# Performance work log

Measured on AMD Instinct MI355X. Metric: run time of the kernel, lower is better.

## Reference

```python
import jax, jax.numpy as jnp
import numpy as np

N_PARENTS = 8
CHILDREN_PER_PARENT = 7
N_CHILDREN = N_PARENTS * CHILDREN_PER_PARENT  # 56 leaf classes
TOTAL_NODES = N_PARENTS + N_CHILDREN          # 64
BATCH = 262144


def _build_state_space():
    """Faithful port of generate_state_space for levels==2.

    Row 0 is the all-zero root state; then for each parent, one parent-only
    row, followed by one (parent, child) row per child. Shape [65, 64].
    """
    S = np.zeros((TOTAL_NODES + 1, TOTAL_NODES), dtype=np.float32)
    recorded = np.zeros(TOTAL_NODES)
    ii = 1
    for c in range(N_CHILDREN):
        p = N_CHILDREN + c // CHILDREN_PER_PARENT  # parent ids 56..63
        if recorded[p] == 0:
            S[ii, p] = 1.0
            recorded[p] = 1
            ii += 1
        S[ii, p] = 1.0
        S[ii, c] = 1.0
        ii += 1
    assert ii == TOTAL_NODES + 1, 'Invalid State Space'
    return jnp.asarray(S)


def setup_inputs() -> dict:
    key = jax.random.key(0)
    k1, k2 = jax.random.split(key)
    pred_label = jax.random.normal(k1, (BATCH, TOTAL_NODES), dtype=jnp.float32)
    gt_label = jax.random.randint(k2, (BATCH,), 0, N_CHILDREN, dtype=jnp.int32)
    return {
        'pred_label': pred_label,
        'gt_label': gt_label,
        'state_space': _build_state_space(),
    }


def reference(pred_label, gt_label, state_space):
    # index[s, b] = <state_space row s, pred_label[b]>  -> [S+1, B]
    index = state_space @ pred_label.T
    joint = jnp.exp(index)                      # [S+1, B]
    z = jnp.sum(joint, axis=0)                  # [B] partition function
    # Vectorized replacement of the per-sample Python loop:
    # rows of the state space that contain the ground-truth node.
    mask = state_space[:, gt_label] > 0         # [S+1, B]
    marginal = jnp.sum(jnp.where(mask, joint, jnp.zeros((), joint.dtype)), axis=0)  # [B]
    loss = -jnp.log(marginal / z)               # [B]
    return jnp.mean(loss)
```

## Files before the change

### kernel.cpp

```cpp
#include <hip/hip_runtime.h>


#define THREADS 256
#define WROWS   32
#define RPB     (4 * WROWS)
#define STRIDE  68

__device__ __forceinline__ float elem(const float4& v, int j) {
    return j == 0 ? v.x : j == 1 ? v.y : j == 2 ? v.z : v.w;
}

__global__ void __launch_bounds__(THREADS) tree_loss_partial(
    const float* __restrict__ pred,
    const int*   __restrict__ gt,
    float*       __restrict__ partial,
    int rows)
{
    __shared__ float lds[4 * WROWS * STRIDE];
    __shared__ float wsum[4];

    const int t = threadIdx.x;
    const int w = t >> 6;
    const int l = t & 63;
    const int waveRowBase = blockIdx.x * RPB + w * WROWS;
    float* e_base = &lds[w * WROWS * STRIDE];

    const float4* p4 = (const float4*)pred + (size_t)waveRowBase * 16;
    const bool full = (waveRowBase + WROWS <= rows);
    float4 v[8];
    #pragma unroll
    for (int i = 0; i < 8; ++i) {
        const int f = i * 64 + l;
        v[i] = (full || waveRowBase + (f >> 4) < rows)
                 ? p4[f] : make_float4(0.f, 0.f, 0.f, 0.f);
    }
    #pragma unroll
    for (int i = 0; i < 8; ++i) {
        const int f   = i * 64 + l;
        const int row = f >> 4;
        const int c4  = (f & 15) << 2;
        float4 ef;
        ef.x = __expf(v[i].x); ef.y = __expf(v[i].y);
        ef.z = __expf(v[i].z); ef.w = __expf(v[i].w);
        *(float4*)(e_base + row * STRIDE + c4) = ef;
    }

    const int r  = l & 31;
    const int hi = l >> 5;
    const float* e = e_base + r * STRIDE;

    float4 ch[7];
    #pragma unroll
    for (int k = 0; k < 7; ++k)
        ch[k] = *(const float4*)(e + hi * 28 + 4 * k);
    const float4 pv = *(const float4*)(e + 56 + 4 * hi);

    float zh = 0.f;
    #pragma unroll
    for (int p = 0; p < 4; ++p) {
        float s = 1.f;
        #pragma unroll
        for (int c = 0; c < 7; ++c) {
            const int idx = p * 7 + c;
            s += elem(ch[idx >> 2], idx & 3);
        }
        zh += elem(pv, p) * s;
    }
    const float zo = __shfl_xor(zh, 32);

    const int  rowg  = waveRowBase + r;
    const bool valid = (rowg < rows);
    float loss = 0.f;
    if (hi == 0 && valid) {
        const int g = gt[rowg];
        const float z = 1.f + zh + zo;
        const float m = e[g] * e[56 + g / 7];
        loss = __logf(z / m);
    }

    #pragma unroll
    for (int off = 32; off; off >>= 1) loss += __shfl_xor(loss, off);
    if (l == 0) wsum[w] = loss;
    __syncthreads();
    if (t == 0) partial[blockIdx.x] = wsum[0] + wsum[1] + wsum[2] + wsum[3];
}

__global__ void __launch_bounds__(256) tree_loss_final(
    const float* __restrict__ partial, int n,
    float* __restrict__ out, float inv)
{
    float s = 0.0f;
    for (int i = threadIdx.x; i < n; i += 256) s += partial[i];
    #pragma unroll
    for (int off = 32; off; off >>= 1) s += __shfl_xor(s, off);
    __shared__ float w[4];
    const int lane = threadIdx.x & 63;
    const int wv   = threadIdx.x >> 6;
    if (lane == 0) w[wv] = s;
    __syncthreads();
    if (threadIdx.x == 0) out[0] = (w[0] + w[1] + w[2] + w[3]) * inv;
}

extern "C" void kernel_launch(void* const* d_in, const int* in_sizes, int n_in,
                              void* d_out, int out_size, void* d_ws, size_t ws_size,
                              hipStream_t stream) {
    const float* pred = (const float*)d_in[0];
    const int*   gt   = (const int*)d_in[1];
    float* out     = (float*)d_out;
    float* partial = (float*)d_ws;
    const int rows = in_sizes[1];

    const int blocks = (rows + RPB - 1) / RPB;
    tree_loss_partial<<<blocks, THREADS, 0, stream>>>(pred, gt, partial, rows);
    tree_loss_final<<<1, 256, 0, stream>>>(partial, blocks, out, 1.0f / (float)rows);
}
```

Before: 22.00 us.

## Fuse final reduction via last-block atomic counter with grid-stride persistent blocks

Replaces the two-kernel scheme (per-block partials plus a separate final reduction kernel) with a single persistent kernel of 1024 blocks that grid-stride over 32-row tiles. The last block to finish, detected through an atomic counter, sums the partials and writes the mean. This removes one kernel launch and reduces the number of partials, at the cost of a memset before the launch and a serialized tail in the last block. The grid-stride loop also processes tiles serially per wave, which may reduce memory-level parallelism compared to one tile per wave.

Measured after the change: 53.24 us. +142.0%, slower.

```diff
diff --git a/kernel.cpp b/kernel.cpp
--- a/kernel.cpp
+++ b/kernel.cpp
@@ -3,18 +3,20 @@
 
 #define THREADS 256
 #define WROWS   32
-#define RPB     (4 * WROWS)
 #define STRIDE  68
+#define BLOCKS  1024
 
 __device__ __forceinline__ float elem(const float4& v, int j) {
     return j == 0 ? v.x : j == 1 ? v.y : j == 2 ? v.z : v.w;
 }
 
-__global__ void __launch_bounds__(THREADS) tree_loss_partial(
+__global__ void __launch_bounds__(THREADS) tree_loss(
     const float* __restrict__ pred,
     const int*   __restrict__ gt,
     float*       __restrict__ partial,
-    int rows)
+    int*         __restrict__ counter,
+    float*       __restrict__ out,
+    int rows, float inv)
 {
     __shared__ float lds[4 * WROWS * STRIDE];
     __shared__ float wsum[4];
@@ -22,83 +24,93 @@
     const int t = threadIdx.x;
     const int w = t >> 6;
     const int l = t & 63;
-    const int waveRowBase = blockIdx.x * RPB + w * WROWS;
     float* e_base = &lds[w * WROWS * STRIDE];
 
-    const float4* p4 = (const float4*)pred + (size_t)waveRowBase * 16;
-    const bool full = (waveRowBase + WROWS <= rows);
-    float4 v[8];
-    #pragma unroll
-    for (int i = 0; i < 8; ++i) {
-        const int f = i * 64 + l;
-        v[i] = (full || waveRowBase + (f >> 4) < rows)
-                 ? p4[f] : make_float4(0.f, 0.f, 0.f, 0.f);
-    }
-    #pragma unroll
-    for (int i = 0; i < 8; ++i) {
-        const int f   = i * 64 + l;
-        const int row = f >> 4;
-        const int c4  = (f & 15) << 2;
-        float4 ef;
-        ef.x = __expf(v[i].x); ef.y = __expf(v[i].y);
-        ef.z = __expf(v[i].z); ef.w = __expf(v[i].w);
-        *(float4*)(e_base + row * STRIDE + c4) = ef;
-    }
+    const int nwaves = (int)gridDim.x * 4;
+    const int ntiles = (rows + WROWS - 1) / WROWS;
 
-    const int r  = l & 31;
-    const int hi = l >> 5;
-    const float* e = e_base + r * STRIDE;
+    float acc = 0.f;
+    for (int tile = (int)blockIdx.x * 4 + w; tile < ntiles; tile += nwaves) {
+        const int waveRowBase = tile * WROWS;
+        const bool full = (waveRowBase + WROWS <= rows);
 
-    float4 ch[7];
-    #pragma unroll
-    for (int k = 0; k < 7; ++k)
-        ch[k] = *(const float4*)(e + hi * 28 + 4 * k);
-    const float4 pv = *(const float4*)(e + 56 + 4 * hi);
+        const float4* p4 = (const float4*)pred + (size_t)waveRowBase * 16;
+        float4 v[8];
+        #pragma unroll
+        for (int i = 0; i < 8; ++i) {
+            const int f = i * 64 + l;
+            v[i] = (full || waveRowBase + (f >> 4) < rows)
+                     ? p4[f] : make_float4(0.f, 0.f, 0.f, 0.f);
+        }
+        #pragma unroll
+        for (int i = 0; i < 8; ++i) {
+            const int f   = i * 64 + l;
+            const int row = f >> 4;
+            const int c4  = (f & 15) << 2;
+            float4 ef;
+            ef.x = __expf(v[i].x); ef.y = __expf(v[i].y);
+            ef.z = __expf(v[i].z); ef.w = __expf(v[i].w);
+            *(float4*)(e_base + row * STRIDE + c4) = ef;
+        }
 
-    float zh = 0.f;
-    #pragma unroll
-    for (int p = 0; p < 4; ++p) {
-        float s = 1.f;
+        const int r  = l & 31;
+        const int hi = l >> 5;
+        const float* e = e_base + r * STRIDE;
+
+        float4 ch[7];
         #pragma unroll
-        for (int c = 0; c < 7; ++c) {
-            const int idx = p * 7 + c;
-            s += elem(ch[idx >> 2], idx & 3);
+        for (int k = 0; k < 7; ++k)
+            ch[k] = *(const float4*)(e + hi * 28 + 4 * k);
+        const float4 pv = *(const float4*)(e + 56 + 4 * hi);
+
+        float zh = 0.f;
+        #pragma unroll
+        for (int p = 0; p < 4; ++p) {
+            float s = 1.f;
+            #pragma unroll
+            for (int c = 0; c < 7; ++c) {
+                const int idx = p * 7 + c;
+                s += elem(ch[idx >> 2], idx & 3);
+            }
+            zh += elem(pv, p) * s;
         }
-        zh += elem(pv, p) * s;
-    }
-    const float zo = __shfl_xor(zh, 32);
+        const float zo = __shfl_xor(zh, 32);
 
-    const int  rowg  = waveRowBase + r;
-    const bool valid = (rowg < rows);
-    float loss = 0.f;
-    if (hi == 0 && valid) {
-        const int g = gt[rowg];
-        const float z = 1.f + zh + zo;
-        const float m = e[g] * e[56 + g / 7];
-        loss = __logf(z / m);
+        const int  rowg  = waveRowBase + r;
+        const bool valid = (rowg < rows);
+        if (hi == 0 && valid) {
+            const int g = gt[rowg];
+            const float z = 1.f + zh + zo;
+            const float m = e[g] * e[56 + g / 7];
+            acc += __logf(z / m);
+        }
     }
 
     #pragma unroll
-    for (int off = 32; off; off >>= 1) loss += __shfl_xor(loss, off);
-    if (l == 0) wsum[w] = loss;
+    for (int off = 32; off; off >>= 1) acc += __shfl_xor(acc, off);
+    if (l == 0) wsum[w] = acc;
     __syncthreads();
-    if (t == 0) partial[blockIdx.x] = wsum[0] + wsum[1] + wsum[2] + wsum[3];
-}
 
-__global__ void __launch_bounds__(256) tree_loss_final(
-    const float* __restrict__ partial, int n,
-    float* __restrict__ out, float inv)
-{
-    float s = 0.0f;
-    for (int i = threadIdx.x; i < n; i += 256) s += partial[i];
-    #pragma unroll
-    for (int off = 32; off; off >>= 1) s += __shfl_xor(s, off);
-    __shared__ float w[4];
-    const int lane = threadIdx.x & 63;
-    const int wv   = threadIdx.x >> 6;
-    if (lane == 0) w[wv] = s;
-    __syncthreads();
-    if (threadIdx.x == 0) out[0] = (w[0] + w[1] + w[2] + w[3]) * inv;
+    if (w == 0) {
+        int old = 0;
+        if (t == 0) {
+            const float b = wsum[0] + wsum[1] + wsum[2] + wsum[3];
+            __hip_atomic_store(&partial[blockIdx.x], b,
+                               __ATOMIC_RELEASE, __HIP_MEMORY_SCOPE_AGENT);
+            old = __hip_atomic_fetch_add(counter, 1,
+                                         __ATOMIC_ACQ_REL, __HIP_MEMORY_SCOPE_AGENT);
+        }
+        old = __shfl(old, 0);
+        if (old == (int)gridDim.x - 1) {
+            float s = 0.f;
+            for (int i = l; i < (int)gridDim.x; i += 64)
+                s += __hip_atomic_load(&partial[i],
+                                       __ATOMIC_ACQUIRE, __HIP_MEMORY_SCOPE_AGENT);
+            #pragma unroll
+            for (int off = 32; off; off >>= 1) s += __shfl_xor(s, off);
+            if (l == 0) out[0] = s * inv;
+        }
+    }
 }
 
 extern "C" void kernel_launch(void* const* d_in, const int* in_sizes, int n_in,
@@ -106,11 +118,13 @@
                               hipStream_t stream) {
     const float* pred = (const float*)d_in[0];
     const int*   gt   = (const int*)d_in[1];
-    float* out     = (float*)d_out;
-    float* partial = (float*)d_ws;
+    float* out = (float*)d_out;
     const int rows = in_sizes[1];
 
-    const int blocks = (rows + RPB - 1) / RPB;
-    tree_loss_partial<<<blocks, THREADS, 0, stream>>>(pred, gt, partial, rows);
-    tree_loss_final<<<1, 256, 0, stream>>>(partial, blocks, out, 1.0f / (float)rows);
+    float* partial = (float*)d_ws;
+    int*   counter = (int*)((char*)d_ws + 4096);
+
+    hipMemsetAsync(counter, 0, sizeof(int), stream);
+    tree_loss<<<BLOCKS, THREADS, 0, stream>>>(
+        pred, gt, partial, counter, out, rows, 1.0f / (float)rows);
 }
```

## Stage pred tiles straight into swizzled LDS and double-buffer per wave

Applied to the files above, without the earlier changes.

The partial kernel now copies pred rows from global memory straight into LDS with global_load_lds dwordx4. The LDS layout is XOR-swizzled instead of padded, and each wave handles two 32-row tiles, using vmcnt waits so computing the first tile overlaps the second tile's load. The loss is now computed in the log domain (log z minus the two logits), so only the exps needed for z are evaluated after the LDS read. Each wave writes its own partial sum, which removes the block barrier, and the final reduction is widened to 1024 threads to handle four times as many partials. This relies on hand-written waitcnt counts and on the gfx950 LDS-load path being correct. Rows past the end are not loaded and are masked out afterwards.

New measurement: 20.08 us. -8.7%, faster.

```diff
diff --git a/kernel.cpp b/kernel.cpp
--- a/kernel.cpp
+++ b/kernel.cpp
@@ -3,11 +3,65 @@
 
 #define THREADS 256
 #define WROWS   32
-#define RPB     (4 * WROWS)
-#define STRIDE  68
+#define RPB     256
 
 __device__ __forceinline__ float elem(const float4& v, int j) {
     return j == 0 ? v.x : j == 1 ? v.y : j == 2 ? v.z : v.w;
+}
+
+__device__ __forceinline__ void stage_tile(const float* __restrict__ pred,
+                                           int rowBase, float* ldsReg,
+                                           int l, int rows) {
+    #pragma unroll
+    for (int i = 0; i < 8; ++i) {
+        const int f   = i * 64 + l;
+        const int rr  = f >> 4;
+        const int sc  = (f & 15) ^ (rr & 7);
+        const int row = rowBase + rr;
+        if (row < rows) {
+            const float* src = pred + (size_t)row * 64 + sc * 4;
+            __builtin_amdgcn_global_load_lds(
+                (const __attribute__((address_space(1))) float*)src,
+                (__attribute__((address_space(3))) float*)(ldsReg + i * 256),
+                16, 0, 0);
+        }
+    }
+}
+
+__device__ __forceinline__ float compute_half(const float* ldsReg, int g,
+                                              int r, int hi) {
+    const int x7 = r & 7;
+    const float* rowp = ldsReg + r * 64;
+
+    float4 ch[7];
+    #pragma unroll
+    for (int k = 0; k < 7; ++k) {
+        const int c = (7 * hi + k) ^ x7;
+        ch[k] = *(const float4*)(rowp + c * 4);
+    }
+    const int cp4 = (14 + hi) ^ x7;
+    const float4 pv = *(const float4*)(rowp + cp4 * 4);
+
+    float zh = 0.f;
+    #pragma unroll
+    for (int p = 0; p < 4; ++p) {
+        float s = 1.f;
+        #pragma unroll
+        for (int c = 0; c < 7; ++c) {
+            const int idx = p * 7 + c;
+            s += __expf(elem(ch[idx >> 2], idx & 3));
+        }
+        zh += __expf(elem(pv, p)) * s;
+    }
+    const float zo = __shfl_xor(zh, 32);
+
+    const int cg = (g >> 2) ^ x7;
+    const float xg = rowp[cg * 4 + (g & 3)];
+    const int wp = 56 + g / 7;
+    const int cpg = (wp >> 2) ^ x7;
+    const float xp = rowp[cpg * 4 + (wp & 3)];
+
+    return __logf(1.f + zh + zo) - xg - xp;
 }
 
 __global__ void __launch_bounds__(THREADS) tree_loss_partial(
@@ -16,89 +70,61 @@
     float*       __restrict__ partial,
     int rows)
 {
-    __shared__ float lds[4 * WROWS * STRIDE];
-    __shared__ float wsum[4];
+    __shared__ float lds[4 * 2 * WROWS * 64];
 
-    const int t = threadIdx.x;
-    const int w = t >> 6;
-    const int l = t & 63;
-    const int waveRowBase = blockIdx.x * RPB + w * WROWS;
-    float* e_base = &lds[w * WROWS * STRIDE];
-
-    const float4* p4 = (const float4*)pred + (size_t)waveRowBase * 16;
-    const bool full = (waveRowBase + WROWS <= rows);
-    float4 v[8];
-    #pragma unroll
-    for (int i = 0; i < 8; ++i) {
-        const int f = i * 64 + l;
-        v[i] = (full || waveRowBase + (f >> 4) < rows)
-                 ? p4[f] : make_float4(0.f, 0.f, 0.f, 0.f);
-    }
-    #pragma unroll
-    for (int i = 0; i < 8; ++i) {
-        const int f   = i * 64 + l;
-        const int row = f >> 4;
-        const int c4  = (f & 15) << 2;
-        float4 ef;
-        ef.x = __expf(v[i].x); ef.y = __expf(v[i].y);
-        ef.z = __expf(v[i].z); ef.w = __expf(v[i].w);
-        *(float4*)(e_base + row * STRIDE + c4) = ef;
-    }
-
+    const int t  = threadIdx.x;
+    const int w  = t >> 6;
+    const int l  = t & 63;
     const int r  = l & 31;
     const int hi = l >> 5;
-    const float* e = e_base + r * STRIDE;
 
-    float4 ch[7];
-    #pragma unroll
-    for (int k = 0; k < 7; ++k)
-        ch[k] = *(const float4*)(e + hi * 28 + 4 * k);
-    const float4 pv = *(const float4*)(e + 56 + 4 * hi);
+    float* regA = &lds[(w * 2 + 0) * WROWS * 64];
+    float* regB = &lds[(w * 2 + 1) * WROWS * 64];
 
-    float zh = 0.f;
-    #pragma unroll
-    for (int p = 0; p < 4; ++p) {
-        float s = 1.f;
-        #pragma unroll
-        for (int c = 0; c < 7; ++c) {
-            const int idx = p * 7 + c;
-            s += elem(ch[idx >> 2], idx & 3);
-        }
-        zh += elem(pv, p) * s;
-    }
-    const float zo = __shfl_xor(zh, 32);
+    const int rbA = (int)blockIdx.x * RPB + w * 64;
+    const int rbB = rbA + WROWS;
+    const int rowA = rbA + r, rowB = rbB + r;
 
-    const int  rowg  = waveRowBase + r;
-    const bool valid = (rowg < rows);
-    float loss = 0.f;
-    if (hi == 0 && valid) {
-        const int g = gt[rowg];
-        const float z = 1.f + zh + zo;
-        const float m = e[g] * e[56 + g / 7];
-        loss = __logf(z / m);
-    }
+    const int gA = gt[min(rowA, rows - 1)];
+    const int gB = gt[min(rowB, rows - 1)];
+
+    stage_tile(pred, rbA, regA, l, rows);
+    stage_tile(pred, rbB, regB, l, rows);
+
+    asm volatile("s_waitcnt vmcnt(8)" ::: "memory");
+    const float lossA = compute_half(regA, gA, r, hi);
+
+    asm volatile("s_waitcnt vmcnt(0)" ::: "memory");
+    const float lossB = compute_half(regB, gB, r, hi);
+
+    float acc = 0.f;
+    if (hi == 0 && rowA < rows) acc += lossA;
+    if (hi == 0 && rowB < rows) acc += lossB;
 
     #pragma unroll
-    for (int off = 32; off; off >>= 1) loss += __shfl_xor(loss, off);
-    if (l == 0) wsum[w] = loss;
-    __syncthreads();
-    if (t == 0) partial[blockIdx.x] = wsum[0] + wsum[1] + wsum[2] + wsum[3];
+    for (int off = 32; off; off >>= 1) acc += __shfl_xor(acc, off);
+    if (l == 0) partial[(size_t)blockIdx.x * 4 + w] = acc;
 }
 
-__global__ void __launch_bounds__(256) tree_loss_final(
+__global__ void __launch_bounds__(1024) tree_loss_final(
     const float* __restrict__ partial, int n,
     float* __restrict__ out, float inv)
 {
     float s = 0.0f;
-    for (int i = threadIdx.x; i < n; i += 256) s += partial[i];
+    for (int i = threadIdx.x; i < n; i += 1024) s += partial[i];
     #pragma unroll
     for (int off = 32; off; off >>= 1) s += __shfl_xor(s, off);
-    __shared__ float w[4];
+    __shared__ float w[16];
     const int lane = threadIdx.x & 63;
     const int wv   = threadIdx.x >> 6;
     if (lane == 0) w[wv] = s;
     __syncthreads();
-    if (threadIdx.x == 0) out[0] = (w[0] + w[1] + w[2] + w[3]) * inv;
+    if (threadIdx.x == 0) {
+        float b = 0.f;
+        #pragma unroll
+        for (int k = 0; k < 16; ++k) b += w[k];
+        out[0] = b * inv;
+    }
 }
 
 extern "C" void kernel_launch(void* const* d_in, const int* in_sizes, int n_in,
@@ -112,5 +138,6 @@
 
     const int blocks = (rows + RPB - 1) / RPB;
     tree_loss_partial<<<blocks, THREADS, 0, stream>>>(pred, gt, partial, rows);
-    tree_loss_final<<<1, 256, 0, stream>>>(partial, blocks, out, 1.0f / (float)rows);
+    tree_loss_final<<<1, 1024, 0, stream>>>(partial, blocks * 4, out,
+                                            1.0f / (float)rows);
 }
```
